# Optimization experiments

Measured on AMD Instinct MI355X. Metric: run time of the kernel, lower is better.

Reference implementation:

```python
import jax, jax.numpy as jnp
import numpy as np

N_WIRES = 6
DIM = 1 << N_WIRES  # 64, equals input channel dim C for amplitude encoding
HID = N_WIRES       # hidden_dim = len(ops)


def _rx(theta):
    c = jnp.cos(theta / 2).astype(jnp.complex64)
    s = jnp.sin(theta / 2).astype(jnp.complex64)
    return jnp.stack([jnp.stack([c, -1j * s]), jnp.stack([-1j * s, c])])


def _ry(theta):
    c = jnp.cos(theta / 2).astype(jnp.complex64)
    s = jnp.sin(theta / 2).astype(jnp.complex64)
    return jnp.stack([jnp.stack([c, -s]), jnp.stack([s, c])])


def _apply_1q(state, U, wire):
    # state: (N, 2, 2, ..., 2); apply 2x2 U on qubit axis wire+1
    s = jnp.moveaxis(state, wire + 1, 1)
    s = jnp.einsum('ab,nb...->na...', U, s)
    return jnp.moveaxis(s, 1, wire + 1)


def _apply_cnot(state, c, t):
    # flip target axis where control bit == 1
    s = jnp.moveaxis(state, (c + 1, t + 1), (1, 2))
    s = jnp.concatenate([s[:, :1], jnp.flip(s[:, 1:2], axis=2)], axis=1)
    return jnp.moveaxis(s, (1, 2), (c + 1, t + 1))


def _expval_z(state, wire):
    # <Z_wire> = P(bit=0) - P(bit=1)
    p = state.real ** 2 + state.imag ** 2
    p = jnp.moveaxis(p, wire + 1, 1).reshape(p.shape[0], 2, -1)
    return p[:, 0].sum(-1) - p[:, 1].sum(-1)


def _value_layer(x_flat, params, qk):
    # amplitude encoding: normalize input into state amplitudes (C == DIM)
    norm = jnp.linalg.norm(x_flat, axis=-1, keepdims=True)
    psi = (x_flat / norm).astype(jnp.complex64)
    state = psi.reshape((x_flat.shape[0],) + (2,) * N_WIRES)
    rx0, ry0, ry1 = params[0], params[1], params[2]
    for j in range(N_WIRES):
        state = _apply_1q(state, _rx(rx0[j]), j)
        state = _apply_1q(state, _ry(ry0[j]), j)
    for j in range(N_WIRES):
        state = _apply_cnot(state, j, (j + 1) % N_WIRES)
    for j in range(N_WIRES):
        state = _apply_1q(state, _ry(ry1[j]), j)
    if qk:
        z0 = _expval_z(state, 0)
        return jnp.stack([z0] * HID, axis=-1)  # qk=True replicates wire-0 <Z>
    return jnp.stack([_expval_z(state, w) for w in range(N_WIRES)], axis=-1)


def setup_inputs() -> dict:
    key = jax.random.key(0)
    k1, k2, k3, k4 = jax.random.split(key, 4)
    B, T, C = 16, 2048, DIM
    return {
        'x': jax.random.normal(k1, (B, T, C), dtype=jnp.float32),
        'params_q': jax.random.normal(k2, (3, N_WIRES), dtype=jnp.float32),
        'params_k': jax.random.normal(k3, (3, N_WIRES), dtype=jnp.float32),
        'params_v': jax.random.normal(k4, (3, N_WIRES), dtype=jnp.float32),
    }


def reference(x, params_q, params_k, params_v):
    B, T, C = x.shape
    xf = x.reshape(B * T, C)
    q = _value_layer(xf, params_q, True).reshape(B, T, HID)
    k = _value_layer(xf, params_k, True).reshape(B, T, HID)
    v = _value_layer(xf, params_v, False).reshape(B, T, HID)
    scores = jnp.einsum('btd,bsd->bts', q, k) / jnp.sqrt(jnp.float32(HID))
    attn = jax.nn.softmax(scores, axis=-1)
    return jnp.einsum('bts,bsd->btd', attn, v)
```

## Files before the change

### kernel.cpp

```cpp
#include <hip/hip_runtime.h>
#include <math.h>

#define NWIRES 6
#define DIM 64
#define NTOK 32768
#define NBATCH 16
#define TPB 2048
#define NMOM 16
#define SQRT6F 2.4494897427831781f
#define APAD 76

typedef short bf16x8 __attribute__((ext_vector_type(8)));
typedef float f32x4  __attribute__((ext_vector_type(4)));

__device__ __forceinline__ unsigned f2bfbits(float f) {
    unsigned u = __float_as_uint(f);
    return (u + 0x7FFF + ((u >> 16) & 1)) >> 16;
}
__device__ __forceinline__ float bfbits2f(unsigned b) {
    return __uint_as_float(b << 16);
}
__device__ __forceinline__ float pswap(float v) { return __shfl_xor(v, 1, 64); }

__global__ __attribute__((amdgpu_waves_per_eu(1, 4)))
__launch_bounds__(256) void qsa_sim(
        const float* __restrict__ x,
        const float* __restrict__ pq,
        const float* __restrict__ pk,
        const float* __restrict__ pv,
        float* __restrict__ zq,
        float* __restrict__ kv) {
    __shared__ unsigned short sAh[128 * APAD];
    __shared__ unsigned short sAl[128 * APAD];
    __shared__ float sTc[64], sTs[64], sP[24];
    int tid = threadIdx.x;
    int tbase = blockIdx.x * 256;
    int circ = blockIdx.y;
    const float* p = (circ == 0) ? pq : (circ == 1 ? pk : pv);

    int lane = tid & 63, wv = tid >> 6;
    int q4 = lane >> 4, c16 = lane & 15;
    int mytok0 = wv * 64 + 0 * 16 + c16;
    const float* xr0 = x + ((size_t)(tbase + mytok0)) * 64;
    float4 rw[4];
#pragma unroll
    for (int ks = 0; ks < 2; ++ks) {
        rw[ks * 2 + 0] = *(const float4*)(xr0 + ks * 32 + q4 * 8);
        rw[ks * 2 + 1] = *(const float4*)(xr0 + ks * 32 + q4 * 8 + 4);
    }

    if (tid < 64) {
        int b = tid;
        float d = 0.f;
#pragma unroll
        for (int j = 0; j < 6; ++j)
            d += 0.5f * p[j] * ((b & (32 >> j)) ? -1.f : 1.f);
        float sd, cd;
        sincosf(d, &sd, &cd);
        sTc[b] = cd;
        sTs[b] = sd;
        if (b < 12) {
            float s, cc;
            sincosf(0.5f * p[6 + b], &s, &cc);
            sP[b * 2 + 0] = cc;
            sP[b * 2 + 1] = s;
        }
    }
    __syncthreads();

    {
        int ph = tid >> 7;
        int k  = (tid >> 1) & 63;
        int h  = tid & 1;
        const float* sTx = ph ? sTs : sTc;
        float v[32];
#pragma unroll
        for (int i = 0; i < 32; ++i) {
            int g = h * 32 + i;
            v[i] = (__popc(g & k) & 1) ? -sTx[g] : sTx[g];
        }
#pragma unroll
        for (int i = 0; i < 32; ++i) {
            float pv_ = pswap(v[i]);
            v[i] = h ? (pv_ - v[i]) : (v[i] + pv_);
        }
#pragma unroll
        for (int M = 16; M >= 1; M >>= 1) {
#pragma unroll
            for (int i = 0; i < 32; ++i) {
                if (i & M) continue;
                int j = i | M;
                float a = v[i], b = v[j];
                v[i] = a + b; v[j] = a - b;
            }
        }
#pragma unroll
        for (int layer = 0; layer < 2; ++layer) {
            const float* Pl = sP + layer * 12;
            {
                float c = Pl[0], ss = h ? Pl[1] : -Pl[1];
#pragma unroll
                for (int i = 0; i < 32; ++i) {
                    float pv_ = pswap(v[i]);
                    v[i] = c * v[i] + ss * pv_;
                }
            }
#pragma unroll
            for (int w = 1; w < 6; ++w) {
                int M = 32 >> w;
                float c = Pl[w * 2], s = Pl[w * 2 + 1];
#pragma unroll
                for (int i = 0; i < 32; ++i) {
                    if (i & M) continue;
                    int j = i | M;
                    float a = v[i], b = v[j];
                    v[i] = c * a - s * b;
                    v[j] = s * a + c * b;
                }
            }
            if (layer == 0) {
#pragma unroll
                for (int i = 0; i < 16; ++i) {
                    int j = i | 16;
                    float a = v[i], b = v[j];
                    v[i] = h ? b : a;
                    v[j] = h ? a : b;
                }
#pragma unroll
                for (int w = 1; w < 5; ++w) {
                    int MC = 32 >> w, MT = MC >> 1;
#pragma unroll
                    for (int i = 0; i < 32; ++i) {
                        if (!(i & MC) || (i & MT)) continue;
                        int j = i | MT;
                        float t = v[i]; v[i] = v[j]; v[j] = t;
                    }
                }
#pragma unroll
                for (int i = 1; i < 32; i += 2) v[i] = pswap(v[i]);
            }
        }
#pragma unroll
        for (int i = 0; i < 32; ++i) {
            int row = ph * 64 + h * 32 + i;
            unsigned hb = f2bfbits(v[i]);
            unsigned lb = f2bfbits(v[i] - bfbits2f(hb));
            sAh[row * APAD + k] = (unsigned short)hb;
            sAl[row * APAD + k] = (unsigned short)lb;
        }
    }
    __syncthreads();

    bf16x8 xh[2], xl[2];
#pragma unroll 1
    for (int cg = 0; cg < 4; ++cg) {
#pragma unroll
        for (int ks = 0; ks < 2; ++ks) {
            float4 f0 = rw[ks * 2], f1 = rw[ks * 2 + 1];
            float ff[8] = {f0.x, f0.y, f0.z, f0.w, f1.x, f1.y, f1.z, f1.w};
#pragma unroll
            for (int e = 0; e < 8; ++e) {
                unsigned hb = f2bfbits(ff[e]);
                unsigned lb = f2bfbits(ff[e] - bfbits2f(hb));
                xh[ks][e] = (short)hb;
                xl[ks][e] = (short)lb;
            }
        }
        int mytok = wv * 64 + cg * 16 + c16;
        if (cg < 3) {
            const float* xrn = x + ((size_t)(tbase + mytok + 16)) * 64;
#pragma unroll
            for (int ks = 0; ks < 2; ++ks) {
                rw[ks * 2 + 0] = *(const float4*)(xrn + ks * 32 + q4 * 8);
                rw[ks * 2 + 1] = *(const float4*)(xrn + ks * 32 + q4 * 8 + 4);
            }
        }

        f32x4 acc[8];
#pragma unroll
        for (int mt = 0; mt < 8; ++mt) acc[mt] = (f32x4){0.f, 0.f, 0.f, 0.f};
#pragma unroll
        for (int mt = 0; mt < 8; ++mt) {
            int r = mt * 16 + c16;
#pragma unroll
            for (int ks = 0; ks < 2; ++ks) {
                const uint2* ph_ = (const uint2*)(&sAh[r * APAD + ks * 32 + q4 * 8]);
                const uint2* pl_ = (const uint2*)(&sAl[r * APAD + ks * 32 + q4 * 8]);
                union { uint2 u[2]; bf16x8 v; } ua, ub;
                ua.u[0] = ph_[0]; ua.u[1] = ph_[1];
                ub.u[0] = pl_[0]; ub.u[1] = pl_[1];
                bf16x8 ah = ua.v, al = ub.v;
                acc[mt] = __builtin_amdgcn_mfma_f32_16x16x32_bf16(ah, xh[ks], acc[mt], 0, 0, 0);
                acc[mt] = __builtin_amdgcn_mfma_f32_16x16x32_bf16(ah, xl[ks], acc[mt], 0, 0, 0);
                acc[mt] = __builtin_amdgcn_mfma_f32_16x16x32_bf16(al, xh[ks], acc[mt], 0, 0, 0);
            }
        }

        float n = 0.f, s0 = 0.f, s1 = 0.f, s2 = 0.f, s3 = 0.f, s4 = 0.f, s5 = 0.f;
        float f2 = (q4 < 2) ? 1.f : 0.f;
        float f3 = (q4 & 1) ? 0.f : 1.f;
#pragma unroll
        for (int mt = 0; mt < 4; ++mt) {
#pragma unroll
            for (int rg = 0; rg < 4; ++rg) {
                float dc = acc[mt][rg];
                float ds = acc[mt + 4][rg];
                float pp = dc * dc + ds * ds;
                n += pp;
                if (!(mt & 2)) s0 += pp;
                if (!(mt & 1)) s1 += pp;
                s2 += f2 * pp;
                s3 += f3 * pp;
                if (!(rg & 2)) s4 += pp;
                if (!(rg & 1)) s5 += pp;
            }
        }
#pragma unroll
        for (int d = 16; d <= 32; d <<= 1) {
            n  += __shfl_xor(n,  d, 64);
            s0 += __shfl_xor(s0, d, 64);
            s1 += __shfl_xor(s1, d, 64);
            s2 += __shfl_xor(s2, d, 64);
            s3 += __shfl_xor(s3, d, 64);
            s4 += __shfl_xor(s4, d, 64);
            s5 += __shfl_xor(s5, d, 64);
        }
        if (q4 == 0) {
            int t = tbase + mytok;
            float inv = 1.0f / n;
            if (circ == 0) {
                zq[t] = SQRT6F * (2.f * s0 - n) * inv;
            } else if (circ == 1) {
                kv[(size_t)t * 8] = (2.f * s0 - n) * inv;
            } else {
                float* o = kv + (size_t)t * 8;
                o[1] = (2.f*s0 - n) * inv;
                o[2] = (2.f*s1 - n) * inv;
                o[3] = (2.f*s2 - n) * inv;
                o[4] = (2.f*s3 - n) * inv;
                o[5] = (2.f*s4 - n) * inv;
                o[6] = (2.f*s5 - n) * inv;
                o[7] = 0.f;
            }
        }
    }
}

__global__ __attribute__((amdgpu_waves_per_eu(1, 2)))
__launch_bounds__(64) void qsa_moments_partial(
        const float* __restrict__ kv,
        float* __restrict__ mpart) {
    int blk = blockIdx.x;
    int b = blk >> 3, c = blk & 7;
    int lane = threadIdx.x;
    float S[NMOM], H[NMOM][6];
#pragma unroll
    for (int m = 0; m < NMOM; ++m) {
        S[m] = 0.f;
#pragma unroll
        for (int w = 0; w < 6; ++w) H[m][w] = 0.f;
    }
    const float* base = kv + ((size_t)(b * TPB + c * 256)) * 8;
#pragma unroll
    for (int r = 0; r < 4; ++r) {
        const float4* e = (const float4*)(base + (size_t)(r * 64 + lane) * 8);
        float4 e0 = e[0], e1 = e[1];
        float z = e0.x;
        float v0 = e0.y, v1 = e0.z, v2 = e0.w, v3 = e1.x, v4 = e1.y, v5 = e1.z;
        float pw = 1.f;
#pragma unroll
        for (int m = 0; m < NMOM; ++m) {
            S[m] += pw;
            H[m][0] += pw * v0; H[m][1] += pw * v1; H[m][2] += pw * v2;
            H[m][3] += pw * v3; H[m][4] += pw * v4; H[m][5] += pw * v5;
            pw *= z;
        }
    }
#pragma unroll
    for (int d = 32; d >= 1; d >>= 1) {
#pragma unroll
        for (int m = 0; m < NMOM; ++m) {
            S[m] += __shfl_xor(S[m], d, 64);
#pragma unroll
            for (int w = 0; w < 6; ++w) H[m][w] += __shfl_xor(H[m][w], d, 64);
        }
    }
    if (lane == 0) {
        float* o = mpart + (size_t)blk * 112;
#pragma unroll
        for (int m = 0; m < NMOM; ++m) {
            float* om = o + m * 7;
            om[0] = S[m];
            om[1] = H[m][0]; om[2] = H[m][1]; om[3] = H[m][2];
            om[4] = H[m][3]; om[5] = H[m][4]; om[6] = H[m][5];
        }
    }
}

__global__ __launch_bounds__(256) void qsa_eval(
        const float* __restrict__ zq,
        const float* __restrict__ mpart,
        float* __restrict__ out) {
    __shared__ float sm[112];
    int bk = blockIdx.x;
    int b = bk >> 3;
    int tid = threadIdx.x;
    if (tid < 112) {
        float s = 0.f;
#pragma unroll
        for (int c = 0; c < 8; ++c) s += mpart[(size_t)(b * 8 + c) * 112 + tid];
        sm[tid] = s;
    }
    __syncthreads();

    int t = bk * 256 + tid;
    float a = zq[t];
    float den = 0.f, o0 = 0.f, o1 = 0.f, o2 = 0.f, o3 = 0.f, o4 = 0.f, o5 = 0.f;
    float pw = 1.f;
#pragma unroll
    for (int m = 0; m < NMOM; ++m) {
        const float* mm = sm + m * 7;
        den += pw * mm[0];
        o0 += pw * mm[1]; o1 += pw * mm[2]; o2 += pw * mm[3];
        o3 += pw * mm[4]; o4 += pw * mm[5]; o5 += pw * mm[6];
        pw *= a * (1.0f / (m + 1));
    }
    float inv = 1.0f / den;
    float* o = out + (size_t)t * 6;
    float2* o2p = (float2*)o;
    o2p[0] = make_float2(o0 * inv, o1 * inv);
    o2p[1] = make_float2(o2 * inv, o3 * inv);
    o2p[2] = make_float2(o4 * inv, o5 * inv);
}

extern "C" void kernel_launch(void* const* d_in, const int* in_sizes, int n_in,
                              void* d_out, int out_size, void* d_ws, size_t ws_size,
                              hipStream_t stream) {
    const float* x  = (const float*)d_in[0];
    const float* pq = (const float*)d_in[1];
    const float* pk = (const float*)d_in[2];
    const float* pv = (const float*)d_in[3];
    float* w = (float*)d_ws;
    float* zq    = w;
    float* kv    = zq + NTOK;
    float* mpart = kv + NTOK * 8;
    float* out   = (float*)d_out;

    qsa_sim<<<dim3(NTOK / 256, 3), 256, 0, stream>>>(x, pq, pk, pv, zq, kv);
    qsa_moments_partial<<<NBATCH * 8, 64, 0, stream>>>(kv, mpart);
    qsa_eval<<<NTOK / 256, 256, 0, stream>>>(zq, mpart, out);
}
```

Baseline: 85.90 us.

## Precompute circuit matrices once in a build kernel and copy into LDS

Moves the per-block construction of the bf16 hi/lo circuit matrices (Walsh-Hadamard transforms, rotations, CNOT permutations) into a separate 3-block kernel that writes them to workspace. Each sim block then loads the precomputed matrices from global/L2 into shared memory with vector copies. This removes the matrix build that every block previously repeated, at the cost of an extra launch and a serial dependency on a tiny kernel. It also adds a redundant store to o[6].

```diff
diff --git a/kernel.cpp b/kernel.cpp
--- a/kernel.cpp
+++ b/kernel.cpp
@@ -20,34 +20,16 @@
 __device__ __forceinline__ float bfbits2f(unsigned b) {
     return __uint_as_float(b << 16);
 }
-__device__ __forceinline__ float pswap(float v) { return __shfl_xor(v, 1, 64); }
-
-__global__ __attribute__((amdgpu_waves_per_eu(1, 4)))
-__launch_bounds__(256) void qsa_sim(
-        const float* __restrict__ x,
+
+__global__ __launch_bounds__(128) void qsa_build(
         const float* __restrict__ pq,
         const float* __restrict__ pk,
         const float* __restrict__ pv,
-        float* __restrict__ zq,
-        float* __restrict__ kv) {
-    __shared__ unsigned short sAh[128 * APAD];
-    __shared__ unsigned short sAl[128 * APAD];
+        unsigned short* __restrict__ gA) {
     __shared__ float sTc[64], sTs[64], sP[24];
+    int circ = blockIdx.x;
+    const float* p = (circ == 0) ? pq : (circ == 1 ? pk : pv);
     int tid = threadIdx.x;
-    int tbase = blockIdx.x * 256;
-    int circ = blockIdx.y;
-    const float* p = (circ == 0) ? pq : (circ == 1 ? pk : pv);
-
-    int lane = tid & 63, wv = tid >> 6;
-    int q4 = lane >> 4, c16 = lane & 15;
-    int mytok0 = wv * 64 + 0 * 16 + c16;
-    const float* xr0 = x + ((size_t)(tbase + mytok0)) * 64;
-    float4 rw[4];
-#pragma unroll
-    for (int ks = 0; ks < 2; ++ks) {
-        rw[ks * 2 + 0] = *(const float4*)(xr0 + ks * 32 + q4 * 8);
-        rw[ks * 2 + 1] = *(const float4*)(xr0 + ks * 32 + q4 * 8 + 4);
-    }
 
     if (tid < 64) {
         int b = tid;
@@ -68,86 +50,108 @@
     }
     __syncthreads();
 
-    {
-        int ph = tid >> 7;
-        int k  = (tid >> 1) & 63;
-        int h  = tid & 1;
-        const float* sTx = ph ? sTs : sTc;
-        float v[32];
-#pragma unroll
-        for (int i = 0; i < 32; ++i) {
-            int g = h * 32 + i;
-            v[i] = (__popc(g & k) & 1) ? -sTx[g] : sTx[g];
-        }
-#pragma unroll
-        for (int i = 0; i < 32; ++i) {
-            float pv_ = pswap(v[i]);
-            v[i] = h ? (pv_ - v[i]) : (v[i] + pv_);
-        }
-#pragma unroll
-        for (int M = 16; M >= 1; M >>= 1) {
-#pragma unroll
-            for (int i = 0; i < 32; ++i) {
+    int ph = tid >> 6;
+    int k  = tid & 63;
+    const float* sTx = ph ? sTs : sTc;
+    float v[64];
+#pragma unroll
+    for (int g = 0; g < 64; ++g)
+        v[g] = (__popc(g & k) & 1) ? -sTx[g] : sTx[g];
+
+#pragma unroll
+    for (int M = 32; M >= 1; M >>= 1) {
+#pragma unroll
+        for (int i = 0; i < 64; ++i) {
+            if (i & M) continue;
+            int j = i | M;
+            float a = v[i], b = v[j];
+            v[i] = a + b; v[j] = a - b;
+        }
+    }
+
+#pragma unroll
+    for (int layer = 0; layer < 2; ++layer) {
+        const float* Pl = sP + layer * 12;
+#pragma unroll
+        for (int w = 0; w < 6; ++w) {
+            int M = 32 >> w;
+            float c = Pl[w * 2], s = Pl[w * 2 + 1];
+#pragma unroll
+            for (int i = 0; i < 64; ++i) {
                 if (i & M) continue;
                 int j = i | M;
                 float a = v[i], b = v[j];
-                v[i] = a + b; v[j] = a - b;
-            }
-        }
-#pragma unroll
-        for (int layer = 0; layer < 2; ++layer) {
-            const float* Pl = sP + layer * 12;
-            {
-                float c = Pl[0], ss = h ? Pl[1] : -Pl[1];
-#pragma unroll
-                for (int i = 0; i < 32; ++i) {
-                    float pv_ = pswap(v[i]);
-                    v[i] = c * v[i] + ss * pv_;
+                v[i] = c * a - s * b;
+                v[j] = s * a + c * b;
+            }
+        }
+        if (layer == 0) {
+#pragma unroll
+            for (int i = 32; i < 64; ++i) {
+                if (i & 16) continue;
+                int j = i | 16;
+                float t = v[i]; v[i] = v[j]; v[j] = t;
+            }
+#pragma unroll
+            for (int w = 1; w < 5; ++w) {
+                int MC = 32 >> w, MT = MC >> 1;
+#pragma unroll
+                for (int i = 0; i < 64; ++i) {
+                    if (!(i & MC) || (i & MT)) continue;
+                    int j = i | MT;
+                    float t = v[i]; v[i] = v[j]; v[j] = t;
                 }
             }
 #pragma unroll
-            for (int w = 1; w < 6; ++w) {
-                int M = 32 >> w;
-                float c = Pl[w * 2], s = Pl[w * 2 + 1];
-#pragma unroll
-                for (int i = 0; i < 32; ++i) {
-                    if (i & M) continue;
-                    int j = i | M;
-                    float a = v[i], b = v[j];
-                    v[i] = c * a - s * b;
-                    v[j] = s * a + c * b;
-                }
-            }
-            if (layer == 0) {
-#pragma unroll
-                for (int i = 0; i < 16; ++i) {
-                    int j = i | 16;
-                    float a = v[i], b = v[j];
-                    v[i] = h ? b : a;
-                    v[j] = h ? a : b;
-                }
-#pragma unroll
-                for (int w = 1; w < 5; ++w) {
-                    int MC = 32 >> w, MT = MC >> 1;
-#pragma unroll
-                    for (int i = 0; i < 32; ++i) {
-                        if (!(i & MC) || (i & MT)) continue;
-                        int j = i | MT;
-                        float t = v[i]; v[i] = v[j]; v[j] = t;
-                    }
-                }
-#pragma unroll
-                for (int i = 1; i < 32; i += 2) v[i] = pswap(v[i]);
-            }
-        }
-#pragma unroll
-        for (int i = 0; i < 32; ++i) {
-            int row = ph * 64 + h * 32 + i;
-            unsigned hb = f2bfbits(v[i]);
-            unsigned lb = f2bfbits(v[i] - bfbits2f(hb));
-            sAh[row * APAD + k] = (unsigned short)hb;
-            sAl[row * APAD + k] = (unsigned short)lb;
-        }
+            for (int i = 1; i < 32; i += 2) {
+                int j = i | 32;
+                float t = v[i]; v[i] = v[j]; v[j] = t;
+            }
+        }
+    }
+
+    unsigned short* g0 = gA + (size_t)circ * (2 * 128 * APAD);
+#pragma unroll
+    for (int i = 0; i < 64; ++i) {
+        int row = ph * 64 + i;
+        unsigned hb = f2bfbits(v[i]);
+        unsigned lb = f2bfbits(v[i] - bfbits2f(hb));
+        g0[row * APAD + k] = (unsigned short)hb;
+        g0[128 * APAD + row * APAD + k] = (unsigned short)lb;
+    }
+}
+
+__global__ __attribute__((amdgpu_waves_per_eu(1, 4)))
+__launch_bounds__(256) void qsa_sim(
+        const float* __restrict__ x,
+        const unsigned short* __restrict__ gA,
+        float* __restrict__ zq,
+        float* __restrict__ kv) {
+    __shared__ __align__(16) unsigned short sA[2 * 128 * APAD];
+    unsigned short* sAh = sA;
+    unsigned short* sAl = sA + 128 * APAD;
+    int tid = threadIdx.x;
+    int tbase = blockIdx.x * 256;
+    int circ = blockIdx.y;
+
+    int lane = tid & 63, wv = tid >> 6;
+    int q4 = lane >> 4, c16 = lane & 15;
+    int mytok0 = wv * 64 + c16;
+    const float* xr0 = x + ((size_t)(tbase + mytok0)) * 64;
+    float4 rw[4];
+#pragma unroll
+    for (int ks = 0; ks < 2; ++ks) {
+        rw[ks * 2 + 0] = *(const float4*)(xr0 + ks * 32 + q4 * 8);
+        rw[ks * 2 + 1] = *(const float4*)(xr0 + ks * 32 + q4 * 8 + 4);
+    }
+
+    {
+        const uint4* gsrc = (const uint4*)(gA + (size_t)circ * (2 * 128 * APAD));
+        uint4* ldst = (uint4*)sA;
+#pragma unroll
+        for (int c = 0; c < 9; ++c)
+            ldst[tid + c * 256] = gsrc[tid + c * 256];
+        if (tid < 128) ldst[tid + 9 * 256] = gsrc[tid + 9 * 256];
     }
     __syncthreads();
 
@@ -239,6 +243,7 @@
                 o[3] = (2.f*s2 - n) * inv;
                 o[4] = (2.f*s3 - n) * inv;
                 o[5] = (2.f*s4 - n) * inv;
+                o[6] = 0.f;
                 o[6] = (2.f*s5 - n) * inv;
                 o[7] = 0.f;
             }
@@ -344,9 +349,11 @@
     float* zq    = w;
     float* kv    = zq + NTOK;
     float* mpart = kv + NTOK * 8;
+    unsigned short* gA = (unsigned short*)(mpart + NBATCH * 8 * 112);
     float* out   = (float*)d_out;
 
-    qsa_sim<<<dim3(NTOK / 256, 3), 256, 0, stream>>>(x, pq, pk, pv, zq, kv);
+    qsa_build<<<3, 128, 0, stream>>>(pq, pk, pv, gA);
+    qsa_sim<<<dim3(NTOK / 256, 3), 256, 0, stream>>>(x, gA, zq, kv);
     qsa_moments_partial<<<NBATCH * 8, 64, 0, stream>>>(kv, mpart);
     qsa_eval<<<NTOK / 256, 256, 0, stream>>>(zq, mpart, out);
 }
```

After: 88.13 us. 1.03x slower.

## Process two token groups per MFMA pass and reduce moments through shared memory

Applied to the files above, without the earlier changes.

The simulation kernel now converts and multiplies two 16-token groups per iteration. Each LDS load of the circuit matrix fragments feeds MFMAs for both groups, which halves LDS traffic per token and gives the MFMA pipe more independent chains. The cost is double the accumulator and x-register footprint, which may reduce occupancy. The moments kernel also replaces its 112-value butterfly shuffle reduction with a padded shared-memory transpose, after which each lane sums one column.

```diff
diff --git a/kernel.cpp b/kernel.cpp
--- a/kernel.cpp
+++ b/kernel.cpp
@@ -40,13 +40,15 @@
 
     int lane = tid & 63, wv = tid >> 6;
     int q4 = lane >> 4, c16 = lane & 15;
-    int mytok0 = wv * 64 + 0 * 16 + c16;
-    const float* xr0 = x + ((size_t)(tbase + mytok0)) * 64;
-    float4 rw[4];
-#pragma unroll
-    for (int ks = 0; ks < 2; ++ks) {
-        rw[ks * 2 + 0] = *(const float4*)(xr0 + ks * 32 + q4 * 8);
-        rw[ks * 2 + 1] = *(const float4*)(xr0 + ks * 32 + q4 * 8 + 4);
+    float4 rw[8];
+#pragma unroll
+    for (int cg = 0; cg < 2; ++cg) {
+        const float* xr = x + ((size_t)(tbase + wv * 64 + cg * 16 + c16)) * 64;
+#pragma unroll
+        for (int ks = 0; ks < 2; ++ks) {
+            rw[cg * 4 + ks * 2 + 0] = *(const float4*)(xr + ks * 32 + q4 * 8);
+            rw[cg * 4 + ks * 2 + 1] = *(const float4*)(xr + ks * 32 + q4 * 8 + 4);
+        }
     }
 
     if (tid < 64) {
@@ -151,34 +153,42 @@
     }
     __syncthreads();
 
-    bf16x8 xh[2], xl[2];
+    bf16x8 xh[2][2], xl[2][2];
 #pragma unroll 1
-    for (int cg = 0; cg < 4; ++cg) {
-#pragma unroll
-        for (int ks = 0; ks < 2; ++ks) {
-            float4 f0 = rw[ks * 2], f1 = rw[ks * 2 + 1];
-            float ff[8] = {f0.x, f0.y, f0.z, f0.w, f1.x, f1.y, f1.z, f1.w};
-#pragma unroll
-            for (int e = 0; e < 8; ++e) {
-                unsigned hb = f2bfbits(ff[e]);
-                unsigned lb = f2bfbits(ff[e] - bfbits2f(hb));
-                xh[ks][e] = (short)hb;
-                xl[ks][e] = (short)lb;
-            }
-        }
-        int mytok = wv * 64 + cg * 16 + c16;
-        if (cg < 3) {
-            const float* xrn = x + ((size_t)(tbase + mytok + 16)) * 64;
+    for (int pr = 0; pr < 2; ++pr) {
+#pragma unroll
+        for (int cg = 0; cg < 2; ++cg) {
 #pragma unroll
             for (int ks = 0; ks < 2; ++ks) {
-                rw[ks * 2 + 0] = *(const float4*)(xrn + ks * 32 + q4 * 8);
-                rw[ks * 2 + 1] = *(const float4*)(xrn + ks * 32 + q4 * 8 + 4);
-            }
-        }
-
-        f32x4 acc[8];
-#pragma unroll
-        for (int mt = 0; mt < 8; ++mt) acc[mt] = (f32x4){0.f, 0.f, 0.f, 0.f};
+                float4 f0 = rw[cg * 4 + ks * 2], f1 = rw[cg * 4 + ks * 2 + 1];
+                float ff[8] = {f0.x, f0.y, f0.z, f0.w, f1.x, f1.y, f1.z, f1.w};
+#pragma unroll
+                for (int e = 0; e < 8; ++e) {
+                    unsigned hb = f2bfbits(ff[e]);
+                    unsigned lb = f2bfbits(ff[e] - bfbits2f(hb));
+                    xh[cg][ks][e] = (short)hb;
+                    xl[cg][ks][e] = (short)lb;
+                }
+            }
+        }
+        if (pr == 0) {
+#pragma unroll
+            for (int cg = 0; cg < 2; ++cg) {
+                const float* xr = x + ((size_t)(tbase + wv * 64 + (2 + cg) * 16 + c16)) * 64;
+#pragma unroll
+                for (int ks = 0; ks < 2; ++ks) {
+                    rw[cg * 4 + ks * 2 + 0] = *(const float4*)(xr + ks * 32 + q4 * 8);
+                    rw[cg * 4 + ks * 2 + 1] = *(const float4*)(xr + ks * 32 + q4 * 8 + 4);
+                }
+            }
+        }
+
+        f32x4 acc[2][8];
+#pragma unroll
+        for (int cg = 0; cg < 2; ++cg)
+#pragma unroll
+            for (int mt = 0; mt < 8; ++mt) acc[cg][mt] = (f32x4){0.f, 0.f, 0.f, 0.f};
+
 #pragma unroll
         for (int mt = 0; mt < 8; ++mt) {
             int r = mt * 16 + c16;
@@ -190,57 +200,63 @@
                 ua.u[0] = ph_[0]; ua.u[1] = ph_[1];
                 ub.u[0] = pl_[0]; ub.u[1] = pl_[1];
                 bf16x8 ah = ua.v, al = ub.v;
-                acc[mt] = __builtin_amdgcn_mfma_f32_16x16x32_bf16(ah, xh[ks], acc[mt], 0, 0, 0);
-                acc[mt] = __builtin_amdgcn_mfma_f32_16x16x32_bf16(ah, xl[ks], acc[mt], 0, 0, 0);
-                acc[mt] = __builtin_amdgcn_mfma_f32_16x16x32_bf16(al, xh[ks], acc[mt], 0, 0, 0);
-            }
-        }
-
-        float n = 0.f, s0 = 0.f, s1 = 0.f, s2 = 0.f, s3 = 0.f, s4 = 0.f, s5 = 0.f;
-        float f2 = (q4 < 2) ? 1.f : 0.f;
-        float f3 = (q4 & 1) ? 0.f : 1.f;
-#pragma unroll
-        for (int mt = 0; mt < 4; ++mt) {
-#pragma unroll
-            for (int rg = 0; rg < 4; ++rg) {
-                float dc = acc[mt][rg];
-                float ds = acc[mt + 4][rg];
-                float pp = dc * dc + ds * ds;
-                n += pp;
-                if (!(mt & 2)) s0 += pp;
-                if (!(mt & 1)) s1 += pp;
-                s2 += f2 * pp;
-                s3 += f3 * pp;
-                if (!(rg & 2)) s4 += pp;
-                if (!(rg & 1)) s5 += pp;
-            }
-        }
-#pragma unroll
-        for (int d = 16; d <= 32; d <<= 1) {
-            n  += __shfl_xor(n,  d, 64);
-            s0 += __shfl_xor(s0, d, 64);
-            s1 += __shfl_xor(s1, d, 64);
-            s2 += __shfl_xor(s2, d, 64);
-            s3 += __shfl_xor(s3, d, 64);
-            s4 += __shfl_xor(s4, d, 64);
-            s5 += __shfl_xor(s5, d, 64);
-        }
-        if (q4 == 0) {
-            int t = tbase + mytok;
-            float inv = 1.0f / n;
-            if (circ == 0) {
-                zq[t] = SQRT6F * (2.f * s0 - n) * inv;
-            } else if (circ == 1) {
-                kv[(size_t)t * 8] = (2.f * s0 - n) * inv;
-            } else {
-                float* o = kv + (size_t)t * 8;
-                o[1] = (2.f*s0 - n) * inv;
-                o[2] = (2.f*s1 - n) * inv;
-                o[3] = (2.f*s2 - n) * inv;
-                o[4] = (2.f*s3 - n) * inv;
-                o[5] = (2.f*s4 - n) * inv;
-                o[6] = (2.f*s5 - n) * inv;
-                o[7] = 0.f;
+#pragma unroll
+                for (int cg = 0; cg < 2; ++cg) {
+                    acc[cg][mt] = __builtin_amdgcn_mfma_f32_16x16x32_bf16(ah, xh[cg][ks], acc[cg][mt], 0, 0, 0);
+                    acc[cg][mt] = __builtin_amdgcn_mfma_f32_16x16x32_bf16(ah, xl[cg][ks], acc[cg][mt], 0, 0, 0);
+                    acc[cg][mt] = __builtin_amdgcn_mfma_f32_16x16x32_bf16(al, xh[cg][ks], acc[cg][mt], 0, 0, 0);
+                }
+            }
+        }
+
+#pragma unroll
+        for (int cg = 0; cg < 2; ++cg) {
+            float n = 0.f, s0 = 0.f, s1 = 0.f, s2 = 0.f, s3 = 0.f, s4 = 0.f, s5 = 0.f;
+            float f2 = (q4 < 2) ? 1.f : 0.f;
+            float f3 = (q4 & 1) ? 0.f : 1.f;
+#pragma unroll
+            for (int mt = 0; mt < 4; ++mt) {
+#pragma unroll
+                for (int rg = 0; rg < 4; ++rg) {
+                    float dc = acc[cg][mt][rg];
+                    float ds = acc[cg][mt + 4][rg];
+                    float pp = dc * dc + ds * ds;
+                    n += pp;
+                    if (!(mt & 2)) s0 += pp;
+                    if (!(mt & 1)) s1 += pp;
+                    s2 += f2 * pp;
+                    s3 += f3 * pp;
+                    if (!(rg & 2)) s4 += pp;
+                    if (!(rg & 1)) s5 += pp;
+                }
+            }
+#pragma unroll
+            for (int d = 16; d <= 32; d <<= 1) {
+                n  += __shfl_xor(n,  d, 64);
+                s0 += __shfl_xor(s0, d, 64);
+                s1 += __shfl_xor(s1, d, 64);
+                s2 += __shfl_xor(s2, d, 64);
+                s3 += __shfl_xor(s3, d, 64);
+                s4 += __shfl_xor(s4, d, 64);
+                s5 += __shfl_xor(s5, d, 64);
+            }
+            if (q4 == 0) {
+                int t = tbase + wv * 64 + (pr * 2 + cg) * 16 + c16;
+                float inv = 1.0f / n;
+                if (circ == 0) {
+                    zq[t] = SQRT6F * (2.f * s0 - n) * inv;
+                } else if (circ == 1) {
+                    kv[(size_t)t * 8] = (2.f * s0 - n) * inv;
+                } else {
+                    float* o = kv + (size_t)t * 8;
+                    o[1] = (2.f*s0 - n) * inv;
+                    o[2] = (2.f*s1 - n) * inv;
+                    o[3] = (2.f*s2 - n) * inv;
+                    o[4] = (2.f*s3 - n) * inv;
+                    o[5] = (2.f*s4 - n) * inv;
+                    o[6] = (2.f*s5 - n) * inv;
+                    o[7] = 0.f;
+                }
             }
         }
     }
@@ -250,6 +266,7 @@
 __launch_bounds__(64) void qsa_moments_partial(
         const float* __restrict__ kv,
         float* __restrict__ mpart) {
+    __shared__ float sm[64 * 113];
     int blk = blockIdx.x;
     int b = blk >> 3, c = blk & 7;
     int lane = threadIdx.x;
@@ -276,23 +293,23 @@
             pw *= z;
         }
     }
-#pragma unroll
-    for (int d = 32; d >= 1; d >>= 1) {
-#pragma unroll
-        for (int m = 0; m < NMOM; ++m) {
-            S[m] += __shfl_xor(S[m], d, 64);
-#pragma unroll
-            for (int w = 0; w < 6; ++w) H[m][w] += __shfl_xor(H[m][w], d, 64);
-        }
-    }
-    if (lane == 0) {
-        float* o = mpart + (size_t)blk * 112;
-#pragma unroll
-        for (int m = 0; m < NMOM; ++m) {
-            float* om = o + m * 7;
-            om[0] = S[m];
-            om[1] = H[m][0]; om[2] = H[m][1]; om[3] = H[m][2];
-            om[4] = H[m][3]; om[5] = H[m][4]; om[6] = H[m][5];
+    float* row = sm + lane * 113;
+#pragma unroll
+    for (int m = 0; m < NMOM; ++m) {
+        row[m * 7 + 0] = S[m];
+        row[m * 7 + 1] = H[m][0]; row[m * 7 + 2] = H[m][1];
+        row[m * 7 + 3] = H[m][2]; row[m * 7 + 4] = H[m][3];
+        row[m * 7 + 5] = H[m][4]; row[m * 7 + 6] = H[m][5];
+    }
+    __syncthreads();
+#pragma unroll
+    for (int vbase = 0; vbase < 2; ++vbase) {
+        int v = vbase * 64 + lane;
+        if (v < 112) {
+            float s = 0.f;
+#pragma unroll
+            for (int r = 0; r < 64; ++r) s += sm[r * 113 + v];
+            mpart[(size_t)blk * 112 + v] = s;
         }
     }
 }
```

Result: slower. 88.48 us (+3.0%).
